# Kernel tuning notes

Hardware: AMD Instinct MI355X
Metric: run time of the kernel (lower is better)

Reference implementation:

```python
import jax, jax.numpy as jnp
import numpy as np

ALPHA = 0.2  # leaky-relu negative slope
N_NODES = 50000
IN_F = 256
OUT_F = 64
N_EDGES = 1600000


def setup_inputs() -> dict:
    key = jax.random.key(0)
    k1, k2, k3, k4 = jax.random.split(key, 4)
    x = jax.random.normal(k1, (N_NODES, IN_F), dtype=jnp.float32)
    # xavier_normal-ish scales for params
    W = jax.random.normal(k2, (IN_F, OUT_F), dtype=jnp.float32) * (1.414 * (2.0 / (IN_F + OUT_F)) ** 0.5)
    a = jax.random.normal(k3, (1, 2 * OUT_F), dtype=jnp.float32) * (1.414 * (2.0 / (1 + 2 * OUT_F)) ** 0.5)
    edge_index = jax.random.randint(k4, (2, N_EDGES), 0, N_NODES, dtype=jnp.int64)
    return {"x": x, "W": W, "a": a, "edge_index": edge_index}


def reference(x, W, a, edge_index):
    N = x.shape[0]
    src = edge_index[0]  # row index of sparse adjacency (aggregation target)
    dst = edge_index[1]  # column index (neighbor being gathered)
    h = x @ W  # [N, out]
    out_f = h.shape[1]
    # a @ cat(h[src], h[dst]) == (h @ a1)[src] + (h @ a2)[dst]
    a1 = a[0, :out_f]
    a2 = a[0, out_f:]
    s_src = h @ a1  # [N]
    s_dst = h @ a2  # [N]
    score = s_src[src] + s_dst[dst]  # [E]
    edge_e = jnp.exp(-jax.nn.leaky_relu(score, negative_slope=ALPHA))  # [E]
    # e_rowsum[i] = sum_{e: src==i} edge_e[e]
    e_rowsum = jax.ops.segment_sum(edge_e, src, num_segments=N)  # [N]
    # h_prime[i] = sum_{e: src==i} edge_e[e] * h[dst[e]]
    h_prime = jax.ops.segment_sum(edge_e[:, None] * h[dst], src, num_segments=N)  # [N, out]
    h_prime = h_prime / e_rowsum[:, None]
    return jax.nn.elu(h_prime)
```

## Files before the change

### kernel.cpp

```cpp
#include <hip/hip_runtime.h>
#include <hip/hip_bf16.h>
#include <hip/hip_fp16.h>


#define ALPHA 0.2f
#define KDIM 256
#define FDIM 64
#define BIN_CHUNK 4096
#define BUCKET_CAP 4096

typedef __bf16 bf16x8 __attribute__((ext_vector_type(8)));
typedef float f32x4 __attribute__((ext_vector_type(4)));
typedef unsigned int u32;
typedef unsigned short u16;

__global__ __launch_bounds__(256) void gat_wt_kernel(
    const float* __restrict__ W, __hip_bfloat16* __restrict__ w_t,
    int* __restrict__ bcur)
{
    const int t = blockIdx.x * 256 + threadIdx.x;
    if (t < KDIM * FDIM) {
        const int k = t >> 6;
        const int n = t & 63;
        w_t[n * KDIM + k] = __float2bfloat16(W[t]);
    }
    if (t < 1024) bcur[t] = 0;
}

__global__ __launch_bounds__(256) void gat_gemm_bin_kernel(
    const float* __restrict__ x, const __hip_bfloat16* __restrict__ w_tp,
    const float* __restrict__ a, __hip_bfloat16* __restrict__ h_bf,
    float* __restrict__ s_src, float* __restrict__ s_dst,
    const int* __restrict__ srcA, const int* __restrict__ dstA,
    int* __restrict__ bcur, u32* __restrict__ pair,
    int N, int E, int NBU, int NBLK)
{
    __shared__ int hist[1024];
    __shared__ int lcur[1024];

    const int t = threadIdx.x;

    if ((int)blockIdx.x < NBLK) {
        for (int j = t; j < 1024; j += 256) hist[j] = 0;
        __syncthreads();
        const int base = blockIdx.x * BIN_CHUNK;
        const int cnt = min(BIN_CHUNK, E - base);
        for (int i = t; i < cnt; i += 256)
            atomicAdd(&hist[srcA[base + i] >> 6], 1);
        __syncthreads();
        for (int j = t; j < NBU; j += 256) {
            const int v = hist[j];
            lcur[j] = v ? (j * BUCKET_CAP + atomicAdd(&bcur[j], v)) : 0;
        }
        __syncthreads();
        for (int i = t; i < cnt; i += 256) {
            const int s = srcA[base + i];
            const int d = dstA[base + i];
            const int pos = atomicAdd(&lcur[s >> 6], 1);
            pair[pos] = ((u32)(s & 63) << 16) | (u32)d;
        }
        return;
    }

    const int gb = (int)blockIdx.x - NBLK;
    const int lane = t & 63;
    const int wv = t >> 6;
    const int m0 = gb * 128 + wv * 32;
    const int c = lane & 15;
    const int q = lane >> 4;

    const int r0 = m0 + c;
    const int r1 = m0 + 16 + c;
    const float* xp0 = x + (long)(r0 < N ? r0 : N - 1) * KDIM;
    const float* xp1 = x + (long)(r1 < N ? r1 : N - 1) * KDIM;
    const __bf16* wt = (const __bf16*)w_tp;

    f32x4 acc[2][4];
#pragma unroll
    for (int rt = 0; rt < 2; ++rt)
#pragma unroll
        for (int ct = 0; ct < 4; ++ct) acc[rt][ct] = (f32x4){0.f, 0.f, 0.f, 0.f};

#pragma unroll 2
    for (int kc = 0; kc < 8; ++kc) {
        const int k0 = kc * 32 + q * 8;
        const float4 xa0 = *(const float4*)(xp0 + k0);
        const float4 xb0 = *(const float4*)(xp0 + k0 + 4);
        const float4 xa1 = *(const float4*)(xp1 + k0);
        const float4 xb1 = *(const float4*)(xp1 + k0 + 4);
        bf16x8 af0, af1;
        af0[0] = (__bf16)xa0.x; af0[1] = (__bf16)xa0.y;
        af0[2] = (__bf16)xa0.z; af0[3] = (__bf16)xa0.w;
        af0[4] = (__bf16)xb0.x; af0[5] = (__bf16)xb0.y;
        af0[6] = (__bf16)xb0.z; af0[7] = (__bf16)xb0.w;
        af1[0] = (__bf16)xa1.x; af1[1] = (__bf16)xa1.y;
        af1[2] = (__bf16)xa1.z; af1[3] = (__bf16)xa1.w;
        af1[4] = (__bf16)xb1.x; af1[5] = (__bf16)xb1.y;
        af1[6] = (__bf16)xb1.z; af1[7] = (__bf16)xb1.w;
#pragma unroll
        for (int ct = 0; ct < 4; ++ct) {
            const bf16x8 bf = *(const bf16x8*)(wt + (ct * 16 + c) * KDIM + k0);
            acc[0][ct] = __builtin_amdgcn_mfma_f32_16x16x32_bf16(af0, bf, acc[0][ct], 0, 0, 0);
            acc[1][ct] = __builtin_amdgcn_mfma_f32_16x16x32_bf16(af1, bf, acc[1][ct], 0, 0, 0);
        }
    }

    float a1c[4], a2c[4];
#pragma unroll
    for (int ct = 0; ct < 4; ++ct) {
        a1c[ct] = a[ct * 16 + c];
        a2c[ct] = a[FDIM + ct * 16 + c];
    }

#pragma unroll
    for (int rt = 0; rt < 2; ++rt) {
        const int mb = m0 + rt * 16;
        float s1r[4], s2r[4];
#pragma unroll
        for (int reg = 0; reg < 4; ++reg) {
            float s1 = 0.f, s2 = 0.f;
#pragma unroll
            for (int ct = 0; ct < 4; ++ct) {
                s1 += acc[rt][ct][reg] * a1c[ct];
                s2 += acc[rt][ct][reg] * a2c[ct];
            }
            s1r[reg] = s1; s2r[reg] = s2;
        }
#pragma unroll
        for (int off = 1; off < 16; off <<= 1) {
#pragma unroll
            for (int reg = 0; reg < 4; ++reg) {
                s1r[reg] += __shfl_xor(s1r[reg], off);
                s2r[reg] += __shfl_xor(s2r[reg], off);
            }
        }
#pragma unroll
        for (int reg = 0; reg < 4; ++reg) {
            const int row = mb + q * 4 + reg;
            if (row < N) {
#pragma unroll
                for (int ct = 0; ct < 4; ++ct)
                    h_bf[(long)row * FDIM + ct * 16 + c] = __float2bfloat16(acc[rt][ct][reg]);
                if (c == 0) { s_src[row] = s1r[reg]; s_dst[row] = s2r[reg]; }
            }
        }
    }
}

__global__ __launch_bounds__(256) void gat_bsort_kernel(
    const u32* __restrict__ pair, const int* __restrict__ bcur,
    const float* __restrict__ s_src, const float* __restrict__ s_dst,
    int* __restrict__ nstart, int* __restrict__ nend,
    u32* __restrict__ sorted_pk, int N)
{
    __shared__ u32 chunk[BUCKET_CAP];
    __shared__ int cur[64];
    __shared__ float ssl[64];

    const int b = blockIdx.x;
    const int t = threadIdx.x;
    const int s0 = b << 6;
    const int abase = b * BUCKET_CAP;
    const int n = min(bcur[b], BUCKET_CAP);

    if (t < 64) {
        cur[t] = 0;
        ssl[t] = (s0 + t < N) ? s_src[s0 + t] : 0.f;
    }
    __syncthreads();
    for (int i = t; i < n; i += 256) {
        const u32 p = pair[abase + i];
        chunk[i] = p;
        atomicAdd(&cur[p >> 16], 1);
    }
    __syncthreads();
    if (t < 64) {
        const int v = cur[t];
        int incl = v;
#pragma unroll
        for (int off = 1; off < 64; off <<= 1) {
            const int nv = __shfl_up(incl, off);
            if (t >= off) incl += nv;
        }
        const int excl = incl - v;
        if (s0 + t < N) {
            nstart[s0 + t] = abase + excl;
            nend[s0 + t] = abase + excl + v;
        }
        cur[t] = excl;
    }
    __syncthreads();
    for (int i = t; i < n; i += 256) {
        const u32 p = chunk[i];
        const int sl = p >> 16;
        const int d = (int)(p & 0xFFFFu);
        const int slot = atomicAdd(&cur[sl], 1);
        const float sc = ssl[sl] + s_dst[d];
        const float lr = sc > 0.f ? sc : ALPHA * sc;
        const float wgt = __expf(-lr);
        const u32 wh = (u32)__half_as_ushort(__float2half(wgt));
        sorted_pk[abase + slot] = (u32)d | (wh << 16);
    }
}

__global__ __launch_bounds__(256) void gat_gather_kernel(
    const int* __restrict__ nstart, const int* __restrict__ nend,
    const u32* __restrict__ sorted_pk,
    const __hip_bfloat16* __restrict__ h_bf, float* __restrict__ out, int N)
{
    const int node = blockIdx.x * 4 + (threadIdx.x >> 6);
    if (node >= N) return;
    const int lane = threadIdx.x & 63;
    const int q = lane >> 3;
    const int c = lane & 7;

    const int start = nstart[node];
    const int end = nend[node];
    const __bf16* hb = (const __bf16*)h_bf;

    float acc0[8], acc1[8];
#pragma unroll
    for (int j = 0; j < 8; ++j) { acc0[j] = 0.f; acc1[j] = 0.f; }
    float wsum0 = 0.f, wsum1 = 0.f;

    int e = start + q;
    for (; e + 8 < end; e += 16) {
        const u32 p0 = sorted_pk[e];
        const u32 p1 = sorted_pk[e + 8];
        const int d0 = (int)(p0 & 0xFFFFu);
        const int d1 = (int)(p1 & 0xFFFFu);
        const bf16x8 hv0 = *(const bf16x8*)(hb + (long)d0 * FDIM + 8 * c);
        const bf16x8 hv1 = *(const bf16x8*)(hb + (long)d1 * FDIM + 8 * c);
        const float w0 = __half2float(__ushort_as_half((u16)(p0 >> 16)));
        const float w1 = __half2float(__ushort_as_half((u16)(p1 >> 16)));
#pragma unroll
        for (int j = 0; j < 8; ++j) {
            acc0[j] += w0 * (float)hv0[j];
            acc1[j] += w1 * (float)hv1[j];
        }
        wsum0 += w0;
        wsum1 += w1;
    }
    if (e < end) {
        const u32 p0 = sorted_pk[e];
        const int d0 = (int)(p0 & 0xFFFFu);
        const bf16x8 hv0 = *(const bf16x8*)(hb + (long)d0 * FDIM + 8 * c);
        const float w0 = __half2float(__ushort_as_half((u16)(p0 >> 16)));
#pragma unroll
        for (int j = 0; j < 8; ++j) acc0[j] += w0 * (float)hv0[j];
        wsum0 += w0;
    }

    float acc[8];
#pragma unroll
    for (int j = 0; j < 8; ++j) acc[j] = acc0[j] + acc1[j];
    float wsum = wsum0 + wsum1;

#pragma unroll
    for (int off = 8; off < 64; off <<= 1) {
#pragma unroll
        for (int j = 0; j < 8; ++j) acc[j] += __shfl_xor(acc[j], off);
        wsum += __shfl_xor(wsum, off);
    }

    if (q == 0) {
        const float inv = 1.0f / wsum;
        float o[8];
#pragma unroll
        for (int j = 0; j < 8; ++j) {
            const float v = acc[j] * inv;
            o[j] = v > 0.f ? v : expm1f(v);
        }
        float* op = &out[(long)node * FDIM + 8 * c];
        *(float4*)op = make_float4(o[0], o[1], o[2], o[3]);
        *(float4*)(op + 4) = make_float4(o[4], o[5], o[6], o[7]);
    }
}

extern "C" void kernel_launch(void* const* d_in, const int* in_sizes, int n_in,
                              void* d_out, int out_size, void* d_ws, size_t ws_size,
                              hipStream_t stream) {
    const float* x = (const float*)d_in[0];
    const float* W = (const float*)d_in[1];
    const float* a = (const float*)d_in[2];
    const int* ei  = (const int*)d_in[3];

    const int N = in_sizes[0] / KDIM;
    const int E = in_sizes[3] / 2;
    const int NBU = (N + 63) >> 6;
    const int NBLK = (E + BIN_CHUNK - 1) / BIN_CHUNK;
    const int GB = (N + 127) / 128;
    const int* srcA = ei;
    const int* dstA = ei + E;

    __hip_bfloat16* h_bf = (__hip_bfloat16*)d_ws;
    __hip_bfloat16* w_t  = h_bf + (size_t)N * FDIM;
    float* s_src = (float*)(w_t + KDIM * FDIM);
    float* s_dst = s_src + N;
    int* nstart  = (int*)(s_dst + N);
    int* nend    = nstart + N;
    int* bcur    = nend + N;
    u32* pair    = (u32*)(bcur + 1024);
    u32* sorted_pk = pair + (size_t)NBU * BUCKET_CAP;
    float* out   = (float*)d_out;

    gat_wt_kernel<<<dim3((KDIM * FDIM + 255) / 256), dim3(256), 0, stream>>>(
        W, w_t, bcur);

    gat_gemm_bin_kernel<<<dim3(NBLK + GB), dim3(256), 0, stream>>>(
        x, w_t, a, h_bf, s_src, s_dst, srcA, dstA, bcur, pair, N, E, NBU, NBLK);

    gat_bsort_kernel<<<dim3(NBU), dim3(256), 0, stream>>>(
        pair, bcur, s_src, s_dst, nstart, nend, sorted_pk, N);

    gat_gather_kernel<<<dim3((N + 3) / 4), dim3(256), 0, stream>>>(
        nstart, nend, sorted_pk, h_bf, out, N);
}
```

Measured before the change: 176.0 us.

## Fuse bucket sort and neighbor gather into one kernel using LDS

Merges the per-bucket counting sort and the weighted neighbor gather into a single 512-thread kernel. The sorted packed (dst, weight) entries and the per-node start/end offsets stay in shared memory instead of being written to and reread from global memory, and one kernel launch is removed. In exchange, each block now handles the gather for 64 nodes with only 8 waves and uses twice the LDS, which cuts the number of blocks and may lower occupancy and latency hiding for the random h row loads.

```diff
diff --git a/kernel.cpp b/kernel.cpp
--- a/kernel.cpp
+++ b/kernel.cpp
@@ -147,14 +147,16 @@
     }
 }
 
-__global__ __launch_bounds__(256) void gat_bsort_kernel(
+__global__ __launch_bounds__(512) void gat_sortgather_kernel(
     const u32* __restrict__ pair, const int* __restrict__ bcur,
     const float* __restrict__ s_src, const float* __restrict__ s_dst,
-    int* __restrict__ nstart, int* __restrict__ nend,
-    u32* __restrict__ sorted_pk, int N)
+    const __hip_bfloat16* __restrict__ h_bf, float* __restrict__ out, int N)
 {
     __shared__ u32 chunk[BUCKET_CAP];
+    __shared__ u32 slds[BUCKET_CAP];
     __shared__ int cur[64];
+    __shared__ int nst[64];
+    __shared__ int nen[64];
     __shared__ float ssl[64];
 
     const int b = blockIdx.x;
@@ -168,7 +170,7 @@
         ssl[t] = (s0 + t < N) ? s_src[s0 + t] : 0.f;
     }
     __syncthreads();
-    for (int i = t; i < n; i += 256) {
+    for (int i = t; i < n; i += 512) {
         const u32 p = pair[abase + i];
         chunk[i] = p;
         atomicAdd(&cur[p >> 16], 1);
@@ -183,14 +185,12 @@
             if (t >= off) incl += nv;
         }
         const int excl = incl - v;
-        if (s0 + t < N) {
-            nstart[s0 + t] = abase + excl;
-            nend[s0 + t] = abase + excl + v;
-        }
+        nst[t] = excl;
+        nen[t] = excl + v;
         cur[t] = excl;
     }
     __syncthreads();
-    for (int i = t; i < n; i += 256) {
+    for (int i = t; i < n; i += 512) {
         const u32 p = chunk[i];
         const int sl = p >> 16;
         const int d = (int)(p & 0xFFFFu);
@@ -199,81 +199,79 @@
         const float lr = sc > 0.f ? sc : ALPHA * sc;
         const float wgt = __expf(-lr);
         const u32 wh = (u32)__half_as_ushort(__float2half(wgt));
-        sorted_pk[abase + slot] = (u32)d | (wh << 16);
-    }
-}
-
-__global__ __launch_bounds__(256) void gat_gather_kernel(
-    const int* __restrict__ nstart, const int* __restrict__ nend,
-    const u32* __restrict__ sorted_pk,
-    const __hip_bfloat16* __restrict__ h_bf, float* __restrict__ out, int N)
-{
-    const int node = blockIdx.x * 4 + (threadIdx.x >> 6);
-    if (node >= N) return;
-    const int lane = threadIdx.x & 63;
+        slds[slot] = (u32)d | (wh << 16);
+    }
+    __syncthreads();
+
+    const int wv = t >> 6;
+    const int lane = t & 63;
     const int q = lane >> 3;
     const int c = lane & 7;
-
-    const int start = nstart[node];
-    const int end = nend[node];
     const __bf16* hb = (const __bf16*)h_bf;
 
-    float acc0[8], acc1[8];
-#pragma unroll
-    for (int j = 0; j < 8; ++j) { acc0[j] = 0.f; acc1[j] = 0.f; }
-    float wsum0 = 0.f, wsum1 = 0.f;
-
-    int e = start + q;
-    for (; e + 8 < end; e += 16) {
-        const u32 p0 = sorted_pk[e];
-        const u32 p1 = sorted_pk[e + 8];
-        const int d0 = (int)(p0 & 0xFFFFu);
-        const int d1 = (int)(p1 & 0xFFFFu);
-        const bf16x8 hv0 = *(const bf16x8*)(hb + (long)d0 * FDIM + 8 * c);
-        const bf16x8 hv1 = *(const bf16x8*)(hb + (long)d1 * FDIM + 8 * c);
-        const float w0 = __half2float(__ushort_as_half((u16)(p0 >> 16)));
-        const float w1 = __half2float(__ushort_as_half((u16)(p1 >> 16)));
-#pragma unroll
-        for (int j = 0; j < 8; ++j) {
-            acc0[j] += w0 * (float)hv0[j];
-            acc1[j] += w1 * (float)hv1[j];
-        }
-        wsum0 += w0;
-        wsum1 += w1;
-    }
-    if (e < end) {
-        const u32 p0 = sorted_pk[e];
-        const int d0 = (int)(p0 & 0xFFFFu);
-        const bf16x8 hv0 = *(const bf16x8*)(hb + (long)d0 * FDIM + 8 * c);
-        const float w0 = __half2float(__ushort_as_half((u16)(p0 >> 16)));
-#pragma unroll
-        for (int j = 0; j < 8; ++j) acc0[j] += w0 * (float)hv0[j];
-        wsum0 += w0;
-    }
-
-    float acc[8];
-#pragma unroll
-    for (int j = 0; j < 8; ++j) acc[j] = acc0[j] + acc1[j];
-    float wsum = wsum0 + wsum1;
-
-#pragma unroll
-    for (int off = 8; off < 64; off <<= 1) {
-#pragma unroll
-        for (int j = 0; j < 8; ++j) acc[j] += __shfl_xor(acc[j], off);
-        wsum += __shfl_xor(wsum, off);
-    }
-
-    if (q == 0) {
-        const float inv = 1.0f / wsum;
-        float o[8];
-#pragma unroll
-        for (int j = 0; j < 8; ++j) {
-            const float v = acc[j] * inv;
-            o[j] = v > 0.f ? v : expm1f(v);
-        }
-        float* op = &out[(long)node * FDIM + 8 * c];
-        *(float4*)op = make_float4(o[0], o[1], o[2], o[3]);
-        *(float4*)(op + 4) = make_float4(o[4], o[5], o[6], o[7]);
+    for (int nl = wv; nl < 64; nl += 8) {
+        const int node = s0 + nl;
+        if (node >= N) break;
+        const int start = nst[nl];
+        const int end = nen[nl];
+
+        float acc0[8], acc1[8];
+#pragma unroll
+        for (int j = 0; j < 8; ++j) { acc0[j] = 0.f; acc1[j] = 0.f; }
+        float wsum0 = 0.f, wsum1 = 0.f;
+
+        int e = start + q;
+        for (; e + 8 < end; e += 16) {
+            const u32 p0 = slds[e];
+            const u32 p1 = slds[e + 8];
+            const int d0 = (int)(p0 & 0xFFFFu);
+            const int d1 = (int)(p1 & 0xFFFFu);
+            const bf16x8 hv0 = *(const bf16x8*)(hb + (long)d0 * FDIM + 8 * c);
+            const bf16x8 hv1 = *(const bf16x8*)(hb + (long)d1 * FDIM + 8 * c);
+            const float w0 = __half2float(__ushort_as_half((u16)(p0 >> 16)));
+            const float w1 = __half2float(__ushort_as_half((u16)(p1 >> 16)));
+#pragma unroll
+            for (int j = 0; j < 8; ++j) {
+                acc0[j] += w0 * (float)hv0[j];
+                acc1[j] += w1 * (float)hv1[j];
+            }
+            wsum0 += w0;
+            wsum1 += w1;
+        }
+        if (e < end) {
+            const u32 p0 = slds[e];
+            const int d0 = (int)(p0 & 0xFFFFu);
+            const bf16x8 hv0 = *(const bf16x8*)(hb + (long)d0 * FDIM + 8 * c);
+            const float w0 = __half2float(__ushort_as_half((u16)(p0 >> 16)));
+#pragma unroll
+            for (int j = 0; j < 8; ++j) acc0[j] += w0 * (float)hv0[j];
+            wsum0 += w0;
+        }
+
+        float acc[8];
+#pragma unroll
+        for (int j = 0; j < 8; ++j) acc[j] = acc0[j] + acc1[j];
+        float wsum = wsum0 + wsum1;
+
+#pragma unroll
+        for (int off = 8; off < 64; off <<= 1) {
+#pragma unroll
+            for (int j = 0; j < 8; ++j) acc[j] += __shfl_xor(acc[j], off);
+            wsum += __shfl_xor(wsum, off);
+        }
+
+        if (q == 0) {
+            const float inv = 1.0f / wsum;
+            float o[8];
+#pragma unroll
+            for (int j = 0; j < 8; ++j) {
+                const float v = acc[j] * inv;
+                o[j] = v > 0.f ? v : expm1f(v);
+            }
+            float* op = &out[(long)node * FDIM + 8 * c];
+            *(float4*)op = make_float4(o[0], o[1], o[2], o[3]);
+            *(float4*)(op + 4) = make_float4(o[4], o[5], o[6], o[7]);
+        }
     }
 }
 
@@ -297,11 +295,8 @@
     __hip_bfloat16* w_t  = h_bf + (size_t)N * FDIM;
     float* s_src = (float*)(w_t + KDIM * FDIM);
     float* s_dst = s_src + N;
-    int* nstart  = (int*)(s_dst + N);
-    int* nend    = nstart + N;
-    int* bcur    = nend + N;
+    int* bcur    = (int*)(s_dst + N);
     u32* pair    = (u32*)(bcur + 1024);
-    u32* sorted_pk = pair + (size_t)NBU * BUCKET_CAP;
     float* out   = (float*)d_out;
 
     gat_wt_kernel<<<dim3((KDIM * FDIM + 255) / 256), dim3(256), 0, stream>>>(
@@ -310,9 +305,6 @@
     gat_gemm_bin_kernel<<<dim3(NBLK + GB), dim3(256), 0, stream>>>(
         x, w_t, a, h_bf, s_src, s_dst, srcA, dstA, bcur, pair, N, E, NBU, NBLK);
 
-    gat_bsort_kernel<<<dim3(NBU), dim3(256), 0, stream>>>(
-        pair, bcur, s_src, s_dst, nstart, nend, sorted_pk, N);
-
-    gat_gather_kernel<<<dim3((N + 3) / 4), dim3(256), 0, stream>>>(
-        nstart, nend, sorted_pk, h_bf, out, N);
+    gat_sortgather_kernel<<<dim3(NBU), dim3(512), 0, stream>>>(
+        pair, bcur, s_src, s_dst, h_bf, out, N);
 }
```

Measured after the change: 170.0 us. 1.04x faster.
